# Kernel optimization log

Measured on AMD Instinct MI355X. Metric: run time of the kernel, lower is better.

The kernel has to match this reference:

```python
import jax, jax.numpy as jnp
import numpy as np

B, L, D = 32, 1024, 128

def setup_inputs() -> dict:
    key = jax.random.key(0)
    kq, kk, kv, ks = jax.random.split(key, 4)
    Q = jax.random.normal(kq, (B, L, D), dtype=jnp.float32)
    K = jax.random.normal(kk, (B, L, D), dtype=jnp.float32)
    V = jax.random.normal(kv, (B, L, D), dtype=jnp.float32)
    kg_sim = jax.random.uniform(ks, (B, L, L), dtype=jnp.float32)
    scale = jnp.float32(1.0 / np.sqrt(D))
    return {"Q": Q, "K": K, "V": V, "scale": scale, "kg_sim": kg_sim}

def reference(Q, K, V, scale, kg_sim):
    # attention = -1 * (Q @ K^T) * scale   [B, L, L]
    attn = -scale * jnp.einsum('bqd,bkd->bqk', Q, K)
    # attention = -softmax(attention, axis=-1)
    attn = -jax.nn.softmax(attn, axis=-1)
    # beta = softmax(attention * kg_sim, axis=-1)
    beta = jax.nn.softmax(attn * kg_sim, axis=-1)
    # context = beta @ V   [B, L, D]
    return jnp.einsum('bqk,bkd->bqd', beta, V)
```

## Files before the change

### kernel.cpp

```cpp
#include <hip/hip_runtime.h>
#include <hip/hip_bf16.h>

#define L 1024
#define D 128
#define NB 32
#define BQ 16

typedef __attribute__((ext_vector_type(8))) short short8;
typedef __attribute__((ext_vector_type(4))) short short4v;
typedef __attribute__((ext_vector_type(4))) float f32x4;

__device__ __forceinline__ unsigned short f2bf(float f) {
    union { float f; unsigned int u; } x; x.f = f;
    unsigned int r = x.u + 0x7FFF + ((x.u >> 16) & 1);
    return (unsigned short)(r >> 16);
}
__device__ __forceinline__ float bf2f(unsigned short u) {
    union { unsigned int u; float f; } x; x.u = ((unsigned int)u) << 16;
    return x.f;
}

__global__ void prep_kernel(const float* __restrict__ K, const float* __restrict__ V,
                            unsigned short* __restrict__ Kb, unsigned short* __restrict__ Vt) {
    __shared__ unsigned short t[32][40];
    int id = blockIdx.x;
    int tid = threadIdx.x;
    if (id < 2048) {
        size_t base = (size_t)id * 2048 + (size_t)tid * 8;
        float4 a = *(const float4*)(K + base);
        float4 c = *(const float4*)(K + base + 4);
        short8 o;
        o[0] = (short)f2bf(a.x); o[1] = (short)f2bf(a.y);
        o[2] = (short)f2bf(a.z); o[3] = (short)f2bf(a.w);
        o[4] = (short)f2bf(c.x); o[5] = (short)f2bf(c.y);
        o[6] = (short)f2bf(c.z); o[7] = (short)f2bf(c.w);
        *(short8*)(Kb + base) = o;
        return;
    }
    id -= 2048;
    int b = id >> 7;
    int rest = id & 127;
    int kt = rest >> 2, dt = rest & 3;
    int k0 = kt * 32, d0 = dt * 32;

    int kl = tid >> 3, dl4 = (tid & 7) * 4;
    const float* src = V + (((size_t)b * L + (k0 + kl)) * D) + d0 + dl4;
    float4 v = *(const float4*)src;
    t[dl4 + 0][kl] = f2bf(v.x);
    t[dl4 + 1][kl] = f2bf(v.y);
    t[dl4 + 2][kl] = f2bf(v.z);
    t[dl4 + 3][kl] = f2bf(v.w);
    __syncthreads();

    int dl = tid >> 3, kl4 = (tid & 7) * 4;
    unsigned short* dst = Vt + (((size_t)b * D + (d0 + dl)) * L) + k0 + kl4;
    short4v o;
    o[0] = (short)t[dl][kl4 + 0];
    o[1] = (short)t[dl][kl4 + 1];
    o[2] = (short)t[dl][kl4 + 2];
    o[3] = (short)t[dl][kl4 + 3];
    *(short4v*)dst = o;
}

__global__ __launch_bounds__(256, 4)
void attn_kernel(const float* __restrict__ Q, const unsigned short* __restrict__ Kb,
                 const float* __restrict__ scale_p, const float* __restrict__ kg,
                 const unsigned short* __restrict__ Vt, float* __restrict__ out) {
    __shared__ unsigned short S16[BQ * 1032];
    __shared__ float zpart[4][BQ];
    __shared__ float row_scale[BQ];

    const int tid = threadIdx.x;
    const int b  = blockIdx.x >> 6;
    const int q0 = (blockIdx.x & 63) * BQ;
    const float nsc = -scale_p[0];

    const int wave = tid >> 6, lane = tid & 63;
    const int lr = lane & 15;
    const int lg = lane >> 4;
    const int row = tid >> 4, l = tid & 15;

    const float* kgrow = kg + (((size_t)b * L) + q0 + row) * L + l * 4;
    float4 kgv[8];
#pragma unroll
    for (int j = 0; j < 8; j++) kgv[j] = *(const float4*)(kgrow + 64 * j);

    short8 aq[4];
#pragma unroll
    for (int kb = 0; kb < 4; kb++) {
        const float* qp = Q + (((size_t)b * L) + q0 + lr) * D + kb * 32 + lg * 8;
        float4 v0 = *(const float4*)qp;
        float4 v1 = *(const float4*)(qp + 4);
        short8 o;
        o[0] = (short)f2bf(v0.x * nsc); o[1] = (short)f2bf(v0.y * nsc);
        o[2] = (short)f2bf(v0.z * nsc); o[3] = (short)f2bf(v0.w * nsc);
        o[4] = (short)f2bf(v1.x * nsc); o[5] = (short)f2bf(v1.y * nsc);
        o[6] = (short)f2bf(v1.z * nsc); o[7] = (short)f2bf(v1.w * nsc);
        aq[kb] = o;
    }

    f32x4 zp = {0.f, 0.f, 0.f, 0.f};
#pragma unroll 2
    for (int i = 0; i < 16; i++) {
        int ct = wave + i * 4;
        const unsigned short* kp = Kb + (((size_t)b * L) + ct * 16 + lr) * D + lg * 8;
        f32x4 acc = {0.f, 0.f, 0.f, 0.f};
#pragma unroll
        for (int kb = 0; kb < 4; kb++) {
            short8 bf = *(const short8*)(kp + kb * 32);
            acc = __builtin_amdgcn_mfma_f32_16x16x32_bf16(aq[kb], bf, acc, 0, 0, 0);
        }
#pragma unroll
        for (int r = 0; r < 4; r++) {
            float p = __expf(acc[r]);
            S16[(lg * 4 + r) * 1032 + ct * 16 + lr] = f2bf(p);
            zp[r] += p;
        }
    }
#pragma unroll
    for (int m = 1; m < 16; m <<= 1) {
#pragma unroll
        for (int r = 0; r < 4; r++) zp[r] += __shfl_xor(zp[r], m, 64);
    }
    if (lr == 0) {
#pragma unroll
        for (int r = 0; r < 4; r++) zpart[wave][lg * 4 + r] = zp[r];
    }
    __syncthreads();

    const float iz1 = 1.0f / (zpart[0][row] + zpart[1][row] +
                              zpart[2][row] + zpart[3][row]);
    unsigned short* srow = &S16[row * 1032];
    float z2 = 0.f;
#pragma unroll
    for (int j = 0; j < 8; j++) {
        unsigned short* p = &srow[l * 4 + 64 * j];
        short4v v = *(const short4v*)p;
        float4 g = kgv[j];
        float e0 = __expf(-(bf2f((unsigned short)v[0]) * iz1) * g.x);
        float e1 = __expf(-(bf2f((unsigned short)v[1]) * iz1) * g.y);
        float e2 = __expf(-(bf2f((unsigned short)v[2]) * iz1) * g.z);
        float e3 = __expf(-(bf2f((unsigned short)v[3]) * iz1) * g.w);
        z2 += (e0 + e1) + (e2 + e3);
        short4v o; o[0] = (short)f2bf(e0); o[1] = (short)f2bf(e1);
        o[2] = (short)f2bf(e2); o[3] = (short)f2bf(e3);
        *(short4v*)p = o;
    }
#pragma unroll
    for (int j = 8; j < 16; j++) {
        float4 g = *(const float4*)(kgrow + 64 * j);
        unsigned short* p = &srow[l * 4 + 64 * j];
        short4v v = *(const short4v*)p;
        float e0 = __expf(-(bf2f((unsigned short)v[0]) * iz1) * g.x);
        float e1 = __expf(-(bf2f((unsigned short)v[1]) * iz1) * g.y);
        float e2 = __expf(-(bf2f((unsigned short)v[2]) * iz1) * g.z);
        float e3 = __expf(-(bf2f((unsigned short)v[3]) * iz1) * g.w);
        z2 += (e0 + e1) + (e2 + e3);
        short4v o; o[0] = (short)f2bf(e0); o[1] = (short)f2bf(e1);
        o[2] = (short)f2bf(e2); o[3] = (short)f2bf(e3);
        *(short4v*)p = o;
    }
#pragma unroll
    for (int m = 1; m < 16; m <<= 1) z2 += __shfl_xor(z2, m, 64);
    if (l == 0) row_scale[row] = 1.0f / z2;
    __syncthreads();

    const int dt0 = wave * 2;
    f32x4 acc0 = {0.f, 0.f, 0.f, 0.f}, acc1 = {0.f, 0.f, 0.f, 0.f};
    const unsigned short* vt0 = Vt + (((size_t)b * D) + dt0 * 16 + lr) * L + lg * 8;
    const unsigned short* vt1 = vt0 + (size_t)16 * L;
    const unsigned short* brow = &S16[lr * 1032 + lg * 8];
#pragma unroll 8
    for (int kb = 0; kb < 32; kb++) {
        short8 a  = *(const short8*)(brow + kb * 32);
        short8 b0 = *(const short8*)(vt0 + kb * 32);
        short8 b1 = *(const short8*)(vt1 + kb * 32);
        acc0 = __builtin_amdgcn_mfma_f32_16x16x32_bf16(a, b0, acc0, 0, 0, 0);
        acc1 = __builtin_amdgcn_mfma_f32_16x16x32_bf16(a, b1, acc1, 0, 0, 0);
    }
    float* orow = out + (((size_t)b * L) + q0) * D;
#pragma unroll
    for (int r = 0; r < 4; r++) {
        int rq = lg * 4 + r;
        float rs = row_scale[rq];
        orow[(size_t)rq * D + dt0 * 16 + lr]       = acc0[r] * rs;
        orow[(size_t)rq * D + (dt0 + 1) * 16 + lr] = acc1[r] * rs;
    }
}

extern "C" void kernel_launch(void* const* d_in, const int* in_sizes, int n_in,
                              void* d_out, int out_size, void* d_ws, size_t ws_size,
                              hipStream_t stream) {
    const float* Q     = (const float*)d_in[0];
    const float* K     = (const float*)d_in[1];
    const float* V     = (const float*)d_in[2];
    const float* scale = (const float*)d_in[3];
    const float* kg    = (const float*)d_in[4];
    float* out = (float*)d_out;
    unsigned short* Vt = (unsigned short*)d_ws;
    unsigned short* Kb = (unsigned short*)d_ws + (size_t)NB * D * L;

    prep_kernel<<<6144, 256, 0, stream>>>(K, V, Kb, Vt);
    attn_kernel<<<NB * (L / BQ), 256, 0, stream>>>(Q, Kb, scale, kg, Vt, out);
}
```

Baseline: 326.7 us.

## Double attention block to 512 threads and drop kg register prefetch

The attention kernel moves from 4 to 8 waves per block. Each wave now handles half as many score column tiles and one 16-column output tile instead of two, and each second-softmax row is processed by 32 threads instead of 16. The early prefetch of kg_sim into registers is removed, so kg is now loaded inside the second-softmax loop. The aim is more parallelism and latency hiding per 16-row query tile with lower register pressure. The cost is exposed kg load latency and heavier block-wide synchronisation.

```diff
diff --git a/kernel.cpp b/kernel.cpp
--- a/kernel.cpp
+++ b/kernel.cpp
@@ -62,12 +62,12 @@
     *(short4v*)dst = o;
 }
 
-__global__ __launch_bounds__(256, 4)
+__global__ __launch_bounds__(512, 8)
 void attn_kernel(const float* __restrict__ Q, const unsigned short* __restrict__ Kb,
                  const float* __restrict__ scale_p, const float* __restrict__ kg,
                  const unsigned short* __restrict__ Vt, float* __restrict__ out) {
     __shared__ unsigned short S16[BQ * 1032];
-    __shared__ float zpart[4][BQ];
+    __shared__ float zpart[8][BQ];
     __shared__ float row_scale[BQ];
 
     const int tid = threadIdx.x;
@@ -78,12 +78,6 @@
     const int wave = tid >> 6, lane = tid & 63;
     const int lr = lane & 15;
     const int lg = lane >> 4;
-    const int row = tid >> 4, l = tid & 15;
-
-    const float* kgrow = kg + (((size_t)b * L) + q0 + row) * L + l * 4;
-    float4 kgv[8];
-#pragma unroll
-    for (int j = 0; j < 8; j++) kgv[j] = *(const float4*)(kgrow + 64 * j);
 
     short8 aq[4];
 #pragma unroll
@@ -101,8 +95,8 @@
 
     f32x4 zp = {0.f, 0.f, 0.f, 0.f};
 #pragma unroll 2
-    for (int i = 0; i < 16; i++) {
-        int ct = wave + i * 4;
+    for (int i = 0; i < 8; i++) {
+        int ct = wave + i * 8;
         const unsigned short* kp = Kb + (((size_t)b * L) + ct * 16 + lr) * D + lg * 8;
         f32x4 acc = {0.f, 0.f, 0.f, 0.f};
 #pragma unroll
@@ -128,28 +122,18 @@
     }
     __syncthreads();
 
-    const float iz1 = 1.0f / (zpart[0][row] + zpart[1][row] +
-                              zpart[2][row] + zpart[3][row]);
+    const int row = tid >> 5, l = tid & 31;
+    float s1 = 0.f;
+#pragma unroll
+    for (int w = 0; w < 8; w++) s1 += zpart[w][row];
+    const float iz1 = 1.0f / s1;
+    const float* kgrow = kg + (((size_t)b * L) + q0 + row) * L + l * 4;
     unsigned short* srow = &S16[row * 1032];
     float z2 = 0.f;
 #pragma unroll
     for (int j = 0; j < 8; j++) {
-        unsigned short* p = &srow[l * 4 + 64 * j];
-        short4v v = *(const short4v*)p;
-        float4 g = kgv[j];
-        float e0 = __expf(-(bf2f((unsigned short)v[0]) * iz1) * g.x);
-        float e1 = __expf(-(bf2f((unsigned short)v[1]) * iz1) * g.y);
-        float e2 = __expf(-(bf2f((unsigned short)v[2]) * iz1) * g.z);
-        float e3 = __expf(-(bf2f((unsigned short)v[3]) * iz1) * g.w);
-        z2 += (e0 + e1) + (e2 + e3);
-        short4v o; o[0] = (short)f2bf(e0); o[1] = (short)f2bf(e1);
-        o[2] = (short)f2bf(e2); o[3] = (short)f2bf(e3);
-        *(short4v*)p = o;
-    }
-#pragma unroll
-    for (int j = 8; j < 16; j++) {
-        float4 g = *(const float4*)(kgrow + 64 * j);
-        unsigned short* p = &srow[l * 4 + 64 * j];
+        float4 g = *(const float4*)(kgrow + 128 * j);
+        unsigned short* p = &srow[l * 4 + 128 * j];
         short4v v = *(const short4v*)p;
         float e0 = __expf(-(bf2f((unsigned short)v[0]) * iz1) * g.x);
         float e1 = __expf(-(bf2f((unsigned short)v[1]) * iz1) * g.y);
@@ -161,30 +145,25 @@
         *(short4v*)p = o;
     }
 #pragma unroll
-    for (int m = 1; m < 16; m <<= 1) z2 += __shfl_xor(z2, m, 64);
+    for (int m = 1; m < 32; m <<= 1) z2 += __shfl_xor(z2, m, 64);
     if (l == 0) row_scale[row] = 1.0f / z2;
     __syncthreads();
 
-    const int dt0 = wave * 2;
-    f32x4 acc0 = {0.f, 0.f, 0.f, 0.f}, acc1 = {0.f, 0.f, 0.f, 0.f};
-    const unsigned short* vt0 = Vt + (((size_t)b * D) + dt0 * 16 + lr) * L + lg * 8;
-    const unsigned short* vt1 = vt0 + (size_t)16 * L;
+    f32x4 acc = {0.f, 0.f, 0.f, 0.f};
+    const unsigned short* vt = Vt + (((size_t)b * D) + wave * 16 + lr) * L + lg * 8;
     const unsigned short* brow = &S16[lr * 1032 + lg * 8];
-#pragma unroll 8
+#pragma unroll 4
     for (int kb = 0; kb < 32; kb++) {
         short8 a  = *(const short8*)(brow + kb * 32);
-        short8 b0 = *(const short8*)(vt0 + kb * 32);
-        short8 b1 = *(const short8*)(vt1 + kb * 32);
-        acc0 = __builtin_amdgcn_mfma_f32_16x16x32_bf16(a, b0, acc0, 0, 0, 0);
-        acc1 = __builtin_amdgcn_mfma_f32_16x16x32_bf16(a, b1, acc1, 0, 0, 0);
+        short8 b0 = *(const short8*)(vt + kb * 32);
+        acc = __builtin_amdgcn_mfma_f32_16x16x32_bf16(a, b0, acc, 0, 0, 0);
     }
     float* orow = out + (((size_t)b * L) + q0) * D;
 #pragma unroll
     for (int r = 0; r < 4; r++) {
         int rq = lg * 4 + r;
         float rs = row_scale[rq];
-        orow[(size_t)rq * D + dt0 * 16 + lr]       = acc0[r] * rs;
-        orow[(size_t)rq * D + (dt0 + 1) * 16 + lr] = acc1[r] * rs;
+        orow[(size_t)rq * D + wave * 16 + lr] = acc[r] * rs;
     }
 }
 
@@ -201,5 +180,5 @@
     unsigned short* Kb = (unsigned short*)d_ws + (size_t)NB * D * L;
 
     prep_kernel<<<6144, 256, 0, stream>>>(K, V, Kb, Vt);
-    attn_kernel<<<NB * (L / BQ), 256, 0, stream>>>(Q, Kb, scale, kg, Vt, out);
+    attn_kernel<<<NB * (L / BQ), 512, 0, stream>>>(Q, Kb, scale, kg, Vt, out);
 }
```

Result: no change. 332.3 us (+1.7%).
